# Optimization experiments

Measured on AMD Instinct MI355X. Metric: run time of the kernel, lower is better.

Reference implementation:

```python
import jax, jax.numpy as jnp
import numpy as np
from jax import lax

OUT_SCALE = 0.001


def setup_inputs() -> dict:
    key = jax.random.key(0)
    kz, kx = jax.random.split(key)
    z = jax.random.normal(kz, (64, 256, 7, 7), dtype=jnp.float32)
    x = jax.random.normal(kx, (64, 256, 31, 31), dtype=jnp.float32)
    return {"z": z, "x": x}


def reference(z, x):
    # depthwise cross-correlation: each (batch, channel) slice of z is slid
    # over the matching slice of x. Implemented as a grouped conv with
    # feature_group_count = B*C, exactly mirroring torch F.conv2d(groups=B*C).
    B, C, kh, kw = z.shape
    H, W = x.shape[2], x.shape[3]
    x_r = x.reshape(1, B * C, H, W)           # [1, B*C, H, W]
    k_r = z.reshape(B * C, 1, kh, kw)          # [B*C, 1, kh, kw] (OIHW)
    out = lax.conv_general_dilated(
        x_r, k_r,
        window_strides=(1, 1),
        padding="VALID",
        feature_group_count=B * C,
        dimension_numbers=("NCHW", "OIHW", "NCHW"),
    )  # [1, B*C, H-kh+1, W-kw+1]
    out = out.reshape(B, C, out.shape[2], out.shape[3])
    return out * OUT_SCALE
```

## Files before the change

kernel.cpp:

```cpp
#include <hip/hip_runtime.h>


#define KH 7
#define KW 7
#define XH 31
#define XW 31
#define OH 25
#define OW 25
#define NSLICE (64 * 256)
#define SPB 5
#define THREADS 128
#define XSTRIDE 35
#define XSLICE (XH * XSTRIDE)

__global__ __launch_bounds__(THREADS)
void xcorr_dw_kernel(const float* __restrict__ z,
                     const float* __restrict__ x,
                     float* __restrict__ out) {
    const int tid = threadIdx.x;
    const int base_slice = blockIdx.x * SPB;
    const int nsl = min(SPB, NSLICE - base_slice);

    __shared__ float xs[SPB * XSLICE];
    __shared__ float zs[SPB * KH * KW];

    const float* __restrict__ xg = x + (size_t)base_slice * (XH * XW);
    const float* __restrict__ zg = z + (size_t)base_slice * (KH * KW);
    const int nx = nsl * (XH * XW);
    for (int idx = tid; idx < nx; idx += THREADS) {
        const int sl  = idx / (XH * XW);
        const int rem = idx - sl * (XH * XW);
        const int row = rem / XW;
        const int col = rem - row * XW;
        xs[sl * XSLICE + row * XSTRIDE + col] = xg[idx];
    }
    const int nz = nsl * (KH * KW);
    for (int idx = tid; idx < nz; idx += THREADS) zs[idx] = zg[idx];
    __syncthreads();

    const int sl = tid / 25;
    const int tt = tid - sl * 25;
    if (sl < nsl) {
        float zr[KH * KW];
        #pragma unroll
        for (int k = 0; k < KH * KW; ++k) zr[k] = zs[sl * (KH * KW) + k];

        const int oy0 = (tt / 5) * 5;
        const int ox0 = (tt % 5) * 5;
        const float* __restrict__ xsp = &xs[sl * XSLICE + oy0 * XSTRIDE + ox0];

        float acc[5][5] = {};
        #pragma unroll
        for (int r = 0; r < 11; ++r) {
            float xr[11];
            #pragma unroll
            for (int c = 0; c < 11; ++c) xr[c] = xsp[r * XSTRIDE + c];
            #pragma unroll
            for (int a = 0; a < 5; ++a) {
                const int i = r - a;
                if (i >= 0 && i < KH) {
                    #pragma unroll
                    for (int j = 0; j < KW; ++j) {
                        const float w = zr[i * KW + j];
                        #pragma unroll
                        for (int b = 0; b < 5; ++b)
                            acc[a][b] = fmaf(xr[j + b], w, acc[a][b]);
                    }
                }
            }
        }

        float* __restrict__ og =
            out + (size_t)(base_slice + sl) * (OH * OW) + oy0 * OW + ox0;
        #pragma unroll
        for (int a = 0; a < 5; ++a) {
            #pragma unroll
            for (int b = 0; b < 5; ++b)
                og[a * OW + b] = acc[a][b] * 0.001f;
        }
    }
}

extern "C" void kernel_launch(void* const* d_in, const int* in_sizes, int n_in,
                              void* d_out, int out_size, void* d_ws, size_t ws_size,
                              hipStream_t stream) {
    const float* z = (const float*)d_in[0];
    const float* x = (const float*)d_in[1];
    float* out = (float*)d_out;
    const int nblk = (NSLICE + SPB - 1) / SPB;
    xcorr_dw_kernel<<<dim3(nblk), dim3(THREADS), 0, stream>>>(z, x, out);
}
```

Baseline: 126.3 us.

## Store input tiles as bf16 in LDS and compute one output row per thread

Converts x and z to bf16, rounding when loaded into shared memory. This halves the LDS footprint and the number of read instructions, since each 32-bit word now holds two packed values. The thread mapping changes from a 5x5 output tile to a full 25-wide output row per thread, reading whole packed rows. Precision drops to bf16 on the inputs, which may exceed the tolerance. Per-thread data reuse also changes: each x row is now loaded 7 times rather than once per tile row.

```diff
diff --git a/kernel.cpp b/kernel.cpp
--- a/kernel.cpp
+++ b/kernel.cpp
@@ -10,8 +10,10 @@
 #define NSLICE (64 * 256)
 #define SPB 5
 #define THREADS 128
-#define XSTRIDE 35
-#define XSLICE (XH * XSTRIDE)
+#define SEL 34
+#define XSLICE_E (XH * SEL)
+#define XSLICE_W (XSLICE_E / 2)
+#define ROW_W (SEL / 2)
 
 __global__ __launch_bounds__(THREADS)
 void xcorr_dw_kernel(const float* __restrict__ z,
@@ -21,63 +23,70 @@
     const int base_slice = blockIdx.x * SPB;
     const int nsl = min(SPB, NSLICE - base_slice);
 
-    __shared__ float xs[SPB * XSLICE];
-    __shared__ float zs[SPB * KH * KW];
+    __shared__ unsigned short xs[SPB * XSLICE_E];
+    __shared__ unsigned int   z_pk[SPB * 25];
 
     const float* __restrict__ xg = x + (size_t)base_slice * (XH * XW);
     const float* __restrict__ zg = z + (size_t)base_slice * (KH * KW);
+
     const int nx = nsl * (XH * XW);
     for (int idx = tid; idx < nx; idx += THREADS) {
-        const int sl  = idx / (XH * XW);
-        const int rem = idx - sl * (XH * XW);
-        const int row = rem / XW;
-        const int col = rem - row * XW;
-        xs[sl * XSLICE + row * XSTRIDE + col] = xg[idx];
+        const int row = idx / XW;
+        const int el  = idx + 3 * row;
+        const unsigned int u = __float_as_uint(xg[idx]);
+        xs[el] = (unsigned short)((u + 0x8000u) >> 16);
     }
-    const int nz = nsl * (KH * KW);
-    for (int idx = tid; idx < nz; idx += THREADS) zs[idx] = zg[idx];
+    if (tid < SPB * 25) {
+        const int sl = tid / 25;
+        const int k  = tid - sl * 25;
+        if (sl < nsl) {
+            const int g = 2 * tid - sl;
+            const unsigned int ua = __float_as_uint(zg[g]);
+            const unsigned int ub = (k < 24) ? __float_as_uint(zg[g + 1]) : 0u;
+            z_pk[tid] = (((ub + 0x8000u) >> 16) << 16) | ((ua + 0x8000u) >> 16);
+        }
+    }
     __syncthreads();
 
     const int sl = tid / 25;
-    const int tt = tid - sl * 25;
+    const int oy = tid - sl * 25;
     if (sl < nsl) {
-        float zr[KH * KW];
+        unsigned int zp[25];
         #pragma unroll
-        for (int k = 0; k < KH * KW; ++k) zr[k] = zs[sl * (KH * KW) + k];
+        for (int k = 0; k < 25; ++k) zp[k] = z_pk[sl * 25 + k];
 
-        const int oy0 = (tt / 5) * 5;
-        const int ox0 = (tt % 5) * 5;
-        const float* __restrict__ xsp = &xs[sl * XSLICE + oy0 * XSTRIDE + ox0];
+        const unsigned int* __restrict__ xw =
+            (const unsigned int*)xs + sl * XSLICE_W;
 
-        float acc[5][5] = {};
+        float acc[OW] = {};
         #pragma unroll
-        for (int r = 0; r < 11; ++r) {
-            float xr[11];
+        for (int i = 0; i < KH; ++i) {
+            const unsigned int* __restrict__ rw = xw + (oy + i) * ROW_W;
+            unsigned int r[16];
             #pragma unroll
-            for (int c = 0; c < 11; ++c) xr[c] = xsp[r * XSTRIDE + c];
+            for (int k = 0; k < 16; ++k) r[k] = rw[k];
+            float f[32];
             #pragma unroll
-            for (int a = 0; a < 5; ++a) {
-                const int i = r - a;
-                if (i >= 0 && i < KH) {
-                    #pragma unroll
-                    for (int j = 0; j < KW; ++j) {
-                        const float w = zr[i * KW + j];
-                        #pragma unroll
-                        for (int b = 0; b < 5; ++b)
-                            acc[a][b] = fmaf(xr[j + b], w, acc[a][b]);
-                    }
-                }
+            for (int k = 0; k < 16; ++k) {
+                f[2 * k]     = __uint_as_float(r[k] << 16);
+                f[2 * k + 1] = __uint_as_float(r[k] & 0xffff0000u);
+            }
+            #pragma unroll
+            for (int j = 0; j < KW; ++j) {
+                const int zi = i * KW + j;
+                const unsigned int dw = zp[zi >> 1];
+                const float w = __uint_as_float((zi & 1) ? (dw & 0xffff0000u)
+                                                         : (dw << 16));
+                #pragma unroll
+                for (int c = 0; c < OW; ++c)
+                    acc[c] = fmaf(f[c + j], w, acc[c]);
             }
         }
 
         float* __restrict__ og =
-            out + (size_t)(base_slice + sl) * (OH * OW) + oy0 * OW + ox0;
+            out + (size_t)(base_slice + sl) * (OH * OW) + oy * OW;
         #pragma unroll
-        for (int a = 0; a < 5; ++a) {
-            #pragma unroll
-            for (int b = 0; b < 5; ++b)
-                og[a * OW + b] = acc[a][b] * 0.001f;
-        }
+        for (int c = 0; c < OW; ++c) og[c] = acc[c] * 0.001f;
     }
 }
 
```

Measured after the change: 132.9 us. 5.2% more time.
